# Kernel optimization log

Measured on AMD Instinct MI355X. Metric: run time of the kernel, lower is better.

## Reference

```python
import jax, jax.numpy as jnp
import numpy as np

EPS = 1e-5

def _bn_relu_over_batch(x, gamma, beta):
    # x: [..., B, F] where batch axis is -2; per-step training-mode BatchNorm1d
    mu = x.mean(axis=-2, keepdims=True)
    var = ((x - mu) ** 2).mean(axis=-2, keepdims=True)  # biased var (torch BN)
    xn = (x - mu) * jax.lax.rsqrt(var + EPS)
    return jax.nn.relu(xn * gamma + beta)

def setup_inputs() -> dict:
    key = jax.random.key(0)
    ks = jax.random.split(key, 8)
    B, T, D_in, E, C, D_out = 8192, 128, 2, 128, 128, 5
    s = 0.1
    return {
        "inputs": jax.random.normal(ks[0], (B, T, D_in), jnp.float32),
        "W_emb": jax.random.normal(ks[1], (E, D_in), jnp.float32) * s,
        "b_emb": jnp.zeros((E,), jnp.float32),
        "g_emb": jnp.ones((E,), jnp.float32),
        "be_emb": jnp.zeros((E,), jnp.float32),
        "W_ih": jax.random.normal(ks[2], (4 * C, E), jnp.float32) * s,
        "W_hh": jax.random.normal(ks[3], (4 * C, C), jnp.float32) * s,
        "b_ih": jnp.zeros((4 * C,), jnp.float32),
        "b_hh": jnp.zeros((4 * C,), jnp.float32),
        "W_out": jax.random.normal(ks[4], (D_out, C), jnp.float32) * s,
        "b_out": jnp.zeros((D_out,), jnp.float32),
        "g_out": jnp.ones((D_out,), jnp.float32),
        "be_out": jnp.zeros((D_out,), jnp.float32),
    }

def reference(inputs, W_emb, b_emb, g_emb, be_emb, W_ih, W_hh, b_ih, b_hh,
              W_out, b_out, g_out, be_out):
    B, T, _ = inputs.shape
    C = W_hh.shape[1]
    # Input embedding: Linear + per-step BatchNorm (batch stats) + ReLU, vectorized over T
    x = jnp.einsum('btd,ed->bte', inputs, W_emb) + b_emb      # [B,T,E]
    x = jnp.transpose(x, (1, 0, 2))                           # [T,B,E]
    x = _bn_relu_over_batch(x, g_emb, be_emb)                 # BN over batch per step

    def step(carry, xt):
        h, c = carry
        gates = xt @ W_ih.T + b_ih + h @ W_hh.T + b_hh        # [B,4C]
        i, f, g, o = jnp.split(gates, 4, axis=-1)             # torch LSTMCell order
        i = jax.nn.sigmoid(i); f = jax.nn.sigmoid(f)
        g = jnp.tanh(g); o = jax.nn.sigmoid(o)
        c = f * c + i * g
        h = o * jnp.tanh(c)
        return (h, c), h

    h0 = jnp.zeros((B, C), inputs.dtype)
    _, h_all = jax.lax.scan(step, (h0, h0), x)                # [T,B,C]

    # Output embedding: Linear + per-step BatchNorm + ReLU
    y = jnp.einsum('tbc,oc->tbo', h_all, W_out) + b_out       # [T,B,5]
    y = _bn_relu_over_batch(y, g_out, be_out)
    return jnp.transpose(y, (1, 0, 2))                        # [B,T,5]
```

## Files before the change

### kernel.cpp

```cpp
#include <hip/hip_runtime.h>

typedef __attribute__((ext_vector_type(8))) short short8;
typedef __attribute__((ext_vector_type(4))) float floatx4;

#define B_TOT 8192
#define T_STEPS 128
#define E_DIM 128
#define C_DIM 128
#define D_OUT 5
#define BN_EPS 1e-5f

#define WS_FLAG   0u
#define WS_WCAT   256u
#define WS_WOUT   (WS_WCAT + 262144u)
#define WS_A0     (WS_WOUT + 4096u)
#define WS_A1     (WS_A0 + 65536u)
#define WS_CC     (WS_A1 + 65536u)
#define WS_STATS  (WS_CC + 65536u)
#define WS_Y      (WS_STATS + 5120u)

__device__ __forceinline__ float bf2f(unsigned short h){
  return __uint_as_float(((unsigned int)h) << 16);
}
__device__ __forceinline__ unsigned short f2b(float v){
  unsigned int u = __float_as_uint(v);
  u += 0x7FFFu + ((u >> 16) & 1u);
  return (unsigned short)(u >> 16);
}
__device__ __forceinline__ float ldf(const void* p, int i, int bf){
  return bf ? bf2f(((const unsigned short*)p)[i]) : ((const float*)p)[i];
}
__device__ __forceinline__ float fast_sig(float x){
  float e = __builtin_amdgcn_exp2f(-1.4426950408889634f * x);
  return __builtin_amdgcn_rcpf(1.0f + e);
}
__device__ __forceinline__ float fast_tanh(float x){
  float e = __builtin_amdgcn_exp2f(2.8853900817779268f * x);
  return 1.0f - 2.0f * __builtin_amdgcn_rcpf(1.0f + e);
}

__global__ void k_detect(const void* g_emb, int* flag){
  if (threadIdx.x == 0 && blockIdx.x == 0){
    unsigned int u = *(const unsigned int*)g_emb;
    *flag = (u == 0x3F803F80u) ? 1 : 0;
  }
}

__global__ void k_prep(const void* W_ih, const void* W_hh, const void* W_out,
                       unsigned short* wcat, unsigned short* wout, const int* flagp){
  const int bf = *flagp;
  int i = blockIdx.x * 256 + threadIdx.x;
  if (i < 512*256){
    int n = i >> 8, k = i & 255;
    float v = (k < 128) ? ldf(W_ih, n*128 + k, bf) : ldf(W_hh, n*128 + (k-128), bf);
    wcat[i] = f2b(v);
  } else {
    int j = i - 512*256;
    int n = j >> 7, k = j & 127;
    float v = (n < D_OUT) ? ldf(W_out, n*128 + k, bf) : 0.0f;
    wout[j] = f2b(v);
  }
}

__global__ void k_instats(const void* x, const void* W_emb, const void* g_emb, const void* be_emb,
                          float* A0, float* A1, float* Cc, const int* flagp){
  const int bf = *flagp;
  const int t = blockIdx.x, tid = threadIdx.x;
  float s0=0,s1=0,s00=0,s11=0,s01=0;
  for (int b = tid; b < B_TOT; b += 256){
    int base = (b*T_STEPS + t)*2;
    float x0 = ldf(x, base, bf), x1 = ldf(x, base+1, bf);
    s0+=x0; s1+=x1; s00+=x0*x0; s11+=x1*x1; s01+=x0*x1;
  }
  for (int off = 32; off; off >>= 1){
    s0 += __shfl_down(s0, off, 64); s1 += __shfl_down(s1, off, 64);
    s00 += __shfl_down(s00, off, 64); s11 += __shfl_down(s11, off, 64);
    s01 += __shfl_down(s01, off, 64);
  }
  __shared__ float red[4][5];
  int wid = tid >> 6, lane = tid & 63;
  if (lane == 0){ red[wid][0]=s0; red[wid][1]=s1; red[wid][2]=s00; red[wid][3]=s11; red[wid][4]=s01; }
  __syncthreads();
  if (tid < E_DIM){
    float S0 = red[0][0]+red[1][0]+red[2][0]+red[3][0];
    float S1 = red[0][1]+red[1][1]+red[2][1]+red[3][1];
    float S00= red[0][2]+red[1][2]+red[2][2]+red[3][2];
    float S11= red[0][3]+red[1][3]+red[2][3]+red[3][3];
    float S01= red[0][4]+red[1][4]+red[2][4]+red[3][4];
    const float inv = 1.0f / (float)B_TOT;
    float mu0 = S0*inv, mu1 = S1*inv;
    float v00 = S00*inv - mu0*mu0, v11 = S11*inv - mu1*mu1, c01 = S01*inv - mu0*mu1;
    int e = tid;
    float w0 = ldf(W_emb, e*2, bf), w1 = ldf(W_emb, e*2+1, bf);
    float g  = ldf(g_emb, e, bf),  be = ldf(be_emb, e, bf);
    float var = w0*w0*v00 + 2.0f*w0*w1*c01 + w1*w1*v11;
    float rs = rsqrtf(var + BN_EPS);
    float a0 = g*rs*w0, a1 = g*rs*w1;
    A0[t*E_DIM+e] = a0; A1[t*E_DIM+e] = a1;
    Cc[t*E_DIM+e] = be - (a0*mu0 + a1*mu1);
  }
}

__global__ __launch_bounds__(512, 2)
void k_lstm(const void* x, const void* b_ih, const void* b_hh,
            const unsigned short* __restrict__ wcat, const unsigned short* __restrict__ wout,
            const float* __restrict__ A0, const float* __restrict__ A1, const float* __restrict__ Cc,
            float* __restrict__ y_ws, const int* flagp){
  const int bf = *flagp;
  const int tid = threadIdx.x;
  const int wid = tid >> 6, lane = tid & 63;
  const int q = lane >> 4, s = lane & 15;
  const int row0 = blockIdx.x * 32;

  __shared__ unsigned short xh[2][32][264];

  short8 bfr[4][8];
#pragma unroll
  for (int gq = 0; gq < 4; ++gq)
#pragma unroll
    for (int ks = 0; ks < 8; ++ks)
      bfr[gq][ks] = *(const short8*)(wcat + ((wid + 8*gq)*16 + s)*256 + ks*32 + q*8);

  short8 wf[4];
#pragma unroll
  for (int ks = 0; ks < 4; ++ks)
    wf[ks] = *(const short8*)(wout + s*128 + ks*32 + q*8);

  const int ch = 16*wid + s;
  float bias[4];
#pragma unroll
  for (int gq = 0; gq < 4; ++gq)
    bias[gq] = ldf(b_ih, gq*128 + ch, bf) + ldf(b_hh, gq*128 + ch, bf);

  float c_st[2][4] = {{0,0,0,0},{0,0,0,0}};

  const int r_loc = tid >> 4;
  const int e0 = (tid & 15) * 8;

  auto compute_xe = [&](int tt, int buf){
    float x0, x1;
    int xbase = ((row0 + r_loc)*T_STEPS + tt)*2;
    if (bf){ const unsigned short* xp = (const unsigned short*)x;
      x0 = bf2f(xp[xbase]); x1 = bf2f(xp[xbase+1]);
    } else { const float* xp = (const float*)x; x0 = xp[xbase]; x1 = xp[xbase+1]; }
    floatx4 a0a = *(const floatx4*)(A0 + tt*E_DIM + e0);
    floatx4 a0b = *(const floatx4*)(A0 + tt*E_DIM + e0 + 4);
    floatx4 a1a = *(const floatx4*)(A1 + tt*E_DIM + e0);
    floatx4 a1b = *(const floatx4*)(A1 + tt*E_DIM + e0 + 4);
    floatx4 cca = *(const floatx4*)(Cc + tt*E_DIM + e0);
    floatx4 ccb = *(const floatx4*)(Cc + tt*E_DIM + e0 + 4);
    short8 pack;
#pragma unroll
    for (int j = 0; j < 4; ++j){
      float v  = fmaxf(fmaf(a0a[j], x0, fmaf(a1a[j], x1, cca[j])), 0.0f);
      float v2 = fmaxf(fmaf(a0b[j], x0, fmaf(a1b[j], x1, ccb[j])), 0.0f);
      pack[j]   = (short)f2b(v);
      pack[4+j] = (short)f2b(v2);
    }
    *(short8*)&xh[buf][r_loc][e0] = pack;
  };

  compute_xe(0, 0);
  {
    short8 z; 
#pragma unroll
    for (int j = 0; j < 8; ++j) z[j] = 0;
    *(short8*)&xh[0][r_loc][128 + e0] = z;
  }
  __syncthreads();

  for (int t = 0; t < T_STEPS; ++t){
    const int cb = t & 1, nb = cb ^ 1;

    if (wid < 2 && t > 0){
      floatx4 ya = {0,0,0,0};
#pragma unroll
      for (int ks = 0; ks < 4; ++ks){
        short8 a = *(const short8*)&xh[cb][s + 16*wid][128 + ks*32 + q*8];
        ya = __builtin_amdgcn_mfma_f32_16x16x32_bf16(a, wf[ks], ya, 0, 0, 0);
      }
      if (s < D_OUT){
#pragma unroll
        for (int r = 0; r < 4; ++r){
          int row = row0 + 16*wid + q*4 + r;
          y_ws[((t-1)*B_TOT + row)*D_OUT + s] = ya[r];
        }
      }
    }

    floatx4 acc[2][4];
#pragma unroll
    for (int mt = 0; mt < 2; ++mt)
#pragma unroll
      for (int gq = 0; gq < 4; ++gq) acc[mt][gq] = (floatx4){0,0,0,0};
#pragma unroll
    for (int ks = 0; ks < 8; ++ks){
      short8 a0 = *(const short8*)&xh[cb][s][ks*32 + q*8];
      short8 a1 = *(const short8*)&xh[cb][s + 16][ks*32 + q*8];
#pragma unroll
      for (int gq = 0; gq < 4; ++gq){
        acc[0][gq] = __builtin_amdgcn_mfma_f32_16x16x32_bf16(a0, bfr[gq][ks], acc[0][gq], 0, 0, 0);
        acc[1][gq] = __builtin_amdgcn_mfma_f32_16x16x32_bf16(a1, bfr[gq][ks], acc[1][gq], 0, 0, 0);
      }
    }

#pragma unroll
    for (int mt = 0; mt < 2; ++mt){
#pragma unroll
      for (int r = 0; r < 4; ++r){
        float gi = fast_sig (acc[mt][0][r] + bias[0]);
        float gf = fast_sig (acc[mt][1][r] + bias[1]);
        float gg = fast_tanh(acc[mt][2][r] + bias[2]);
        float go = fast_sig (acc[mt][3][r] + bias[3]);
        float cn = gf * c_st[mt][r] + gi * gg;
        c_st[mt][r] = cn;
        float hv = go * fast_tanh(cn);
        xh[nb][16*mt + q*4 + r][128 + ch] = f2b(hv);
      }
    }

    if (t < T_STEPS-1) compute_xe(t+1, nb);
    __syncthreads();
  }

  if (wid < 2){
    floatx4 ya = {0,0,0,0};
#pragma unroll
    for (int ks = 0; ks < 4; ++ks){
      short8 a = *(const short8*)&xh[0][s + 16*wid][128 + ks*32 + q*8];
      ya = __builtin_amdgcn_mfma_f32_16x16x32_bf16(a, wf[ks], ya, 0, 0, 0);
    }
    if (s < D_OUT){
#pragma unroll
      for (int r = 0; r < 4; ++r){
        int row = row0 + 16*wid + q*4 + r;
        y_ws[((T_STEPS-1)*B_TOT + row)*D_OUT + s] = ya[r];
      }
    }
  }
}

__global__ void k_outstats(const float* __restrict__ y_ws, const void* g_out, const void* be_out,
                           float* stats, const int* flagp){
  const int bf = *flagp;
  const int t = blockIdx.x / 5, o = blockIdx.x % 5;
  const int tid = threadIdx.x;
  float s = 0.0f, ss = 0.0f;
  for (int b = tid; b < B_TOT; b += 256){
    float v = y_ws[(t*B_TOT + b)*D_OUT + o];
    s += v; ss += v*v;
  }
  for (int off = 32; off; off >>= 1){ s += __shfl_down(s, off, 64); ss += __shfl_down(ss, off, 64); }
  __shared__ float red[4][2];
  int wid = tid >> 6, lane = tid & 63;
  if (lane == 0){ red[wid][0] = s; red[wid][1] = ss; }
  __syncthreads();
  if (tid == 0){
    float S  = red[0][0]+red[1][0]+red[2][0]+red[3][0];
    float SS = red[0][1]+red[1][1]+red[2][1]+red[3][1];
    const float inv = 1.0f / (float)B_TOT;
    float mu = S*inv, var = SS*inv - mu*mu;
    float g = ldf(g_out, o, bf), be = ldf(be_out, o, bf);
    float sc = g * rsqrtf(var + BN_EPS);
    stats[blockIdx.x*2]   = sc;
    stats[blockIdx.x*2+1] = be - sc*mu;
  }
}

__global__ void k_apply(const float* __restrict__ y_ws, const float* __restrict__ stats,
                        void* out, const int* flagp){
  const int bf = *flagp;
  int i = blockIdx.x*512 + threadIdx.x;
  int b = i / 640;
  int rem = i - b*640;
  int t = rem / 5, o = rem - t*5;
  float v = y_ws[(t*B_TOT + b)*D_OUT + o];
  int si = (t*5 + o)*2;
  v = fmaxf(fmaf(v, stats[si], stats[si+1]), 0.0f);
  if (bf) ((unsigned short*)out)[i] = f2b(v);
  else    ((float*)out)[i] = v;
}

extern "C" void kernel_launch(void* const* d_in, const int* in_sizes, int n_in,
                              void* d_out, int out_size, void* d_ws, size_t ws_size,
                              hipStream_t stream){
  const void* x      = d_in[0];
  const void* W_emb  = d_in[1];
  const void* g_emb  = d_in[3];
  const void* be_emb = d_in[4];
  const void* W_ih   = d_in[5];
  const void* W_hh   = d_in[6];
  const void* b_ih   = d_in[7];
  const void* b_hh   = d_in[8];
  const void* W_out  = d_in[9];
  const void* g_out  = d_in[11];
  const void* be_out = d_in[12];

  char* ws = (char*)d_ws;
  int* flag = (int*)(ws + WS_FLAG);
  unsigned short* wcat = (unsigned short*)(ws + WS_WCAT);
  unsigned short* wout = (unsigned short*)(ws + WS_WOUT);
  float* A0    = (float*)(ws + WS_A0);
  float* A1    = (float*)(ws + WS_A1);
  float* Cc    = (float*)(ws + WS_CC);
  float* stats = (float*)(ws + WS_STATS);
  float* y_ws  = (float*)(ws + WS_Y);

  k_detect  <<<dim3(1),     dim3(64),  0, stream>>>(g_emb, flag);
  k_prep    <<<dim3(520),   dim3(256), 0, stream>>>(W_ih, W_hh, W_out, wcat, wout, flag);
  k_instats <<<dim3(128),   dim3(256), 0, stream>>>(x, W_emb, g_emb, be_emb, A0, A1, Cc, flag);
  k_lstm    <<<dim3(256),   dim3(512), 0, stream>>>(x, b_ih, b_hh, wcat, wout, A0, A1, Cc, y_ws, flag);
  k_outstats<<<dim3(640),   dim3(256), 0, stream>>>(y_ws, g_out, be_out, stats, flag);
  k_apply   <<<dim3(10240), dim3(512), 0, stream>>>(y_ws, stats, d_out, flag);
}
```

Baseline: 466.9 us.

## Coalesce stats and output kernels, prefetch embedding loads, fold bias into accumulators

The input-statistics kernel is split into a coalesced partial-moments kernel and a small coefficient kernel. The output-statistics kernel now reads each timestep's contiguous block once with LDS atomics. The apply kernel transposes through an LDS tile so global reads and writes are coalesced. Inside the LSTM it prefetches the next step's embedding inputs before the MFMAs, folds the gate bias into the accumulator init, uses cheaper bf16 rounding, pads LDS rows and uses a raw waitcnt+barrier, which adds register pressure and slightly changes rounding.

Result: slower. 487.2 us (+4.3%).

```diff
diff --git a/kernel.cpp b/kernel.cpp
--- a/kernel.cpp
+++ b/kernel.cpp
@@ -17,7 +17,8 @@
 #define WS_A1     (WS_A0 + 65536u)
 #define WS_CC     (WS_A1 + 65536u)
 #define WS_STATS  (WS_CC + 65536u)
-#define WS_Y      (WS_STATS + 5120u)
+#define WS_PART   (WS_STATS + 5120u)
+#define WS_Y      (WS_PART + 20480u)
 
 __device__ __forceinline__ float bf2f(unsigned short h){
   return __uint_as_float(((unsigned int)h) << 16);
@@ -27,6 +28,9 @@
   u += 0x7FFFu + ((u >> 16) & 1u);
   return (unsigned short)(u >> 16);
 }
+__device__ __forceinline__ unsigned short f2b_fast(float v){
+  return (unsigned short)((__float_as_uint(v) + 0x8000u) >> 16);
+}
 __device__ __forceinline__ float ldf(const void* p, int i, int bf){
   return bf ? bf2f(((const unsigned short*)p)[i]) : ((const float*)p)[i];
 }
@@ -37,6 +41,9 @@
 __device__ __forceinline__ float fast_tanh(float x){
   float e = __builtin_amdgcn_exp2f(2.8853900817779268f * x);
   return 1.0f - 2.0f * __builtin_amdgcn_rcpf(1.0f + e);
+}
+__device__ __forceinline__ void lds_barrier(){
+  asm volatile("s_waitcnt lgkmcnt(0)\n\ts_barrier" ::: "memory");
 }
 
 __global__ void k_detect(const void* g_emb, int* flag){
@@ -62,43 +69,88 @@
   }
 }
 
-__global__ void k_instats(const void* x, const void* W_emb, const void* g_emb, const void* be_emb,
-                          float* A0, float* A1, float* Cc, const int* flagp){
-  const int bf = *flagp;
-  const int t = blockIdx.x, tid = threadIdx.x;
-  float s0=0,s1=0,s00=0,s11=0,s01=0;
-  for (int b = tid; b < B_TOT; b += 256){
-    int base = (b*T_STEPS + t)*2;
-    float x0 = ldf(x, base, bf), x1 = ldf(x, base+1, bf);
-    s0+=x0; s1+=x1; s00+=x0*x0; s11+=x1*x1; s01+=x0*x1;
-  }
-  for (int off = 32; off; off >>= 1){
-    s0 += __shfl_down(s0, off, 64); s1 += __shfl_down(s1, off, 64);
-    s00 += __shfl_down(s00, off, 64); s11 += __shfl_down(s11, off, 64);
-    s01 += __shfl_down(s01, off, 64);
-  }
-  __shared__ float red[4][5];
-  int wid = tid >> 6, lane = tid & 63;
-  if (lane == 0){ red[wid][0]=s0; red[wid][1]=s1; red[wid][2]=s00; red[wid][3]=s11; red[wid][4]=s01; }
+__global__ void k_moments(const void* x, float* part, const int* flagp){
+  const int bf = *flagp;
+  const int wdw = (blockIdx.x >> 3) * 8;
+  const int rg  = blockIdx.x & 7;
+  const int tid = threadIdx.x;
+  const int wv = tid >> 6, lane = tid & 63;
+  __shared__ float red[8][16][3];
+
+  if (!bf){
+    const float* xp = (const float*)x;
+    const int row_b = tid >> 4, j = tid & 15;
+    float a0=0, a1=0, a2=0;
+    for (int c = 0; c < 32; ++c){
+      int row = rg*1024 + c*32 + row_b;
+      float v = xp[row*256 + wdw*2 + j];
+      float p = __shfl_xor(v, 1, 64);
+      if ((j & 1) == 0){ a0 += v; a1 += v*v; a2 += v*p; }
+      else             { a0 += v; a1 += v*v; }
+    }
+    a0 += __shfl_down(a0,32,64); a0 += __shfl_down(a0,16,64);
+    a1 += __shfl_down(a1,32,64); a1 += __shfl_down(a1,16,64);
+    a2 += __shfl_down(a2,32,64); a2 += __shfl_down(a2,16,64);
+    if (lane < 16){ red[wv][lane][0]=a0; red[wv][lane][1]=a1; red[wv][lane][2]=a2; }
+  } else {
+    const unsigned int* xp = (const unsigned int*)x;
+    const int row_b = tid >> 3, j = tid & 7;
+    float s0=0,s1=0,s00=0,s11=0,s01=0;
+    for (int c = 0; c < 16; ++c){
+      int row = rg*1024 + c*64 + row_b;
+      unsigned int u = xp[row*128 + wdw + j];
+      float xv0 = bf2f((unsigned short)(u & 0xFFFFu));
+      float xv1 = bf2f((unsigned short)(u >> 16));
+      s0+=xv0; s1+=xv1; s00+=xv0*xv0; s11+=xv1*xv1; s01+=xv0*xv1;
+    }
+    s0 += __shfl_down(s0,32,64); s0 += __shfl_down(s0,16,64); s0 += __shfl_down(s0,8,64);
+    s1 += __shfl_down(s1,32,64); s1 += __shfl_down(s1,16,64); s1 += __shfl_down(s1,8,64);
+    s00+= __shfl_down(s00,32,64);s00+= __shfl_down(s00,16,64);s00+= __shfl_down(s00,8,64);
+    s11+= __shfl_down(s11,32,64);s11+= __shfl_down(s11,16,64);s11+= __shfl_down(s11,8,64);
+    s01+= __shfl_down(s01,32,64);s01+= __shfl_down(s01,16,64);s01+= __shfl_down(s01,8,64);
+    if (lane < 8){
+      red[wv][lane][0]=s0;  red[wv][lane][1]=s00; red[wv][lane][2]=s01;
+      red[wv][8+lane][0]=s1; red[wv][8+lane][1]=s11;
+    }
+  }
   __syncthreads();
-  if (tid < E_DIM){
-    float S0 = red[0][0]+red[1][0]+red[2][0]+red[3][0];
-    float S1 = red[0][1]+red[1][1]+red[2][1]+red[3][1];
-    float S00= red[0][2]+red[1][2]+red[2][2]+red[3][2];
-    float S11= red[0][3]+red[1][3]+red[2][3]+red[3][3];
-    float S01= red[0][4]+red[1][4]+red[2][4]+red[3][4];
-    const float inv = 1.0f / (float)B_TOT;
-    float mu0 = S0*inv, mu1 = S1*inv;
-    float v00 = S00*inv - mu0*mu0, v11 = S11*inv - mu1*mu1, c01 = S01*inv - mu0*mu1;
-    int e = tid;
-    float w0 = ldf(W_emb, e*2, bf), w1 = ldf(W_emb, e*2+1, bf);
-    float g  = ldf(g_emb, e, bf),  be = ldf(be_emb, e, bf);
-    float var = w0*w0*v00 + 2.0f*w0*w1*c01 + w1*w1*v11;
-    float rs = rsqrtf(var + BN_EPS);
-    float a0 = g*rs*w0, a1 = g*rs*w1;
-    A0[t*E_DIM+e] = a0; A1[t*E_DIM+e] = a1;
-    Cc[t*E_DIM+e] = be - (a0*mu0 + a1*mu1);
-  }
+  if (tid < 8){
+    int tl = tid;
+    float S0=0,S1=0,S00=0,S11=0,S01=0;
+    for (int w8 = 0; w8 < 8; ++w8){
+      if (!bf){
+        S0 += red[w8][2*tl][0];   S00 += red[w8][2*tl][1];   S01 += red[w8][2*tl][2];
+        S1 += red[w8][2*tl+1][0]; S11 += red[w8][2*tl+1][1];
+      } else {
+        S0 += red[w8][tl][0];     S00 += red[w8][tl][1];     S01 += red[w8][tl][2];
+        S1 += red[w8][8+tl][0];   S11 += red[w8][8+tl][1];
+      }
+    }
+    float* dst = part + rg*640 + (wdw + tl)*5;
+    dst[0]=S0; dst[1]=S1; dst[2]=S00; dst[3]=S11; dst[4]=S01;
+  }
+}
+
+__global__ void k_coef(const float* part, const void* W_emb, const void* g_emb, const void* be_emb,
+                       float* A0, float* A1, float* Cc, const int* flagp){
+  const int bf = *flagp;
+  int i = blockIdx.x*256 + threadIdx.x;
+  int t = i >> 7, e = i & 127;
+  float S0=0,S1=0,S00=0,S11=0,S01=0;
+  for (int rg = 0; rg < 8; ++rg){
+    const float* p = part + rg*640 + t*5;
+    S0+=p[0]; S1+=p[1]; S00+=p[2]; S11+=p[3]; S01+=p[4];
+  }
+  const float inv = 1.0f / (float)B_TOT;
+  float mu0 = S0*inv, mu1 = S1*inv;
+  float v00 = S00*inv - mu0*mu0, v11 = S11*inv - mu1*mu1, c01 = S01*inv - mu0*mu1;
+  float w0 = ldf(W_emb, e*2, bf), w1 = ldf(W_emb, e*2+1, bf);
+  float g  = ldf(g_emb, e, bf),  be = ldf(be_emb, e, bf);
+  float var = w0*w0*v00 + 2.0f*w0*w1*c01 + w1*w1*v11;
+  float rs = rsqrtf(var + BN_EPS);
+  float a0 = g*rs*w0, a1 = g*rs*w1;
+  A0[i] = a0; A1[i] = a1;
+  Cc[i] = be - (a0*mu0 + a1*mu1);
 }
 
 __global__ __launch_bounds__(512, 2)
@@ -112,7 +164,7 @@
   const int q = lane >> 4, s = lane & 15;
   const int row0 = blockIdx.x * 32;
 
-  __shared__ unsigned short xh[2][32][264];
+  __shared__ unsigned short xh[2][32][266];
 
   short8 bfr[4][8];
 #pragma unroll
@@ -127,50 +179,58 @@
     wf[ks] = *(const short8*)(wout + s*128 + ks*32 + q*8);
 
   const int ch = 16*wid + s;
-  float bias[4];
-#pragma unroll
-  for (int gq = 0; gq < 4; ++gq)
-    bias[gq] = ldf(b_ih, gq*128 + ch, bf) + ldf(b_hh, gq*128 + ch, bf);
+  floatx4 binit[4];
+#pragma unroll
+  for (int gq = 0; gq < 4; ++gq){
+    float b = ldf(b_ih, gq*128 + ch, bf) + ldf(b_hh, gq*128 + ch, bf);
+    binit[gq] = (floatx4){b, b, b, b};
+  }
 
   float c_st[2][4] = {{0,0,0,0},{0,0,0,0}};
 
   const int r_loc = tid >> 4;
   const int e0 = (tid & 15) * 8;
 
-  auto compute_xe = [&](int tt, int buf){
-    float x0, x1;
+  float x0p, x1p;
+  floatx4 pA0a, pA0b, pA1a, pA1b, pCa, pCb;
+
+  auto xe_load = [&](int tt){
     int xbase = ((row0 + r_loc)*T_STEPS + tt)*2;
     if (bf){ const unsigned short* xp = (const unsigned short*)x;
-      x0 = bf2f(xp[xbase]); x1 = bf2f(xp[xbase+1]);
-    } else { const float* xp = (const float*)x; x0 = xp[xbase]; x1 = xp[xbase+1]; }
-    floatx4 a0a = *(const floatx4*)(A0 + tt*E_DIM + e0);
-    floatx4 a0b = *(const floatx4*)(A0 + tt*E_DIM + e0 + 4);
-    floatx4 a1a = *(const floatx4*)(A1 + tt*E_DIM + e0);
-    floatx4 a1b = *(const floatx4*)(A1 + tt*E_DIM + e0 + 4);
-    floatx4 cca = *(const floatx4*)(Cc + tt*E_DIM + e0);
-    floatx4 ccb = *(const floatx4*)(Cc + tt*E_DIM + e0 + 4);
+      x0p = bf2f(xp[xbase]); x1p = bf2f(xp[xbase+1]);
+    } else { const float* xp = (const float*)x; x0p = xp[xbase]; x1p = xp[xbase+1]; }
+    pA0a = *(const floatx4*)(A0 + tt*E_DIM + e0);
+    pA0b = *(const floatx4*)(A0 + tt*E_DIM + e0 + 4);
+    pA1a = *(const floatx4*)(A1 + tt*E_DIM + e0);
+    pA1b = *(const floatx4*)(A1 + tt*E_DIM + e0 + 4);
+    pCa  = *(const floatx4*)(Cc + tt*E_DIM + e0);
+    pCb  = *(const floatx4*)(Cc + tt*E_DIM + e0 + 4);
+  };
+  auto xe_store = [&](int buf){
     short8 pack;
 #pragma unroll
     for (int j = 0; j < 4; ++j){
-      float v  = fmaxf(fmaf(a0a[j], x0, fmaf(a1a[j], x1, cca[j])), 0.0f);
-      float v2 = fmaxf(fmaf(a0b[j], x0, fmaf(a1b[j], x1, ccb[j])), 0.0f);
-      pack[j]   = (short)f2b(v);
-      pack[4+j] = (short)f2b(v2);
+      float v  = fmaxf(fmaf(pA0a[j], x0p, fmaf(pA1a[j], x1p, pCa[j])), 0.0f);
+      float v2 = fmaxf(fmaf(pA0b[j], x0p, fmaf(pA1b[j], x1p, pCb[j])), 0.0f);
+      pack[j]   = (short)f2b_fast(v);
+      pack[4+j] = (short)f2b_fast(v2);
     }
     *(short8*)&xh[buf][r_loc][e0] = pack;
   };
 
-  compute_xe(0, 0);
+  xe_load(0); xe_store(0);
   {
-    short8 z; 
+    short8 z;
 #pragma unroll
     for (int j = 0; j < 8; ++j) z[j] = 0;
     *(short8*)&xh[0][r_loc][128 + e0] = z;
   }
-  __syncthreads();
+  lds_barrier();
 
   for (int t = 0; t < T_STEPS; ++t){
     const int cb = t & 1, nb = cb ^ 1;
+
+    if (t < T_STEPS-1) xe_load(t+1);
 
     if (wid < 2 && t > 0){
       floatx4 ya = {0,0,0,0};
@@ -192,7 +252,7 @@
 #pragma unroll
     for (int mt = 0; mt < 2; ++mt)
 #pragma unroll
-      for (int gq = 0; gq < 4; ++gq) acc[mt][gq] = (floatx4){0,0,0,0};
+      for (int gq = 0; gq < 4; ++gq) acc[mt][gq] = binit[gq];
 #pragma unroll
     for (int ks = 0; ks < 8; ++ks){
       short8 a0 = *(const short8*)&xh[cb][s][ks*32 + q*8];
@@ -208,19 +268,19 @@
     for (int mt = 0; mt < 2; ++mt){
 #pragma unroll
       for (int r = 0; r < 4; ++r){
-        float gi = fast_sig (acc[mt][0][r] + bias[0]);
-        float gf = fast_sig (acc[mt][1][r] + bias[1]);
-        float gg = fast_tanh(acc[mt][2][r] + bias[2]);
-        float go = fast_sig (acc[mt][3][r] + bias[3]);
+        float gi = fast_sig (acc[mt][0][r]);
+        float gf = fast_sig (acc[mt][1][r]);
+        float gg = fast_tanh(acc[mt][2][r]);
+        float go = fast_sig (acc[mt][3][r]);
         float cn = gf * c_st[mt][r] + gi * gg;
         c_st[mt][r] = cn;
         float hv = go * fast_tanh(cn);
-        xh[nb][16*mt + q*4 + r][128 + ch] = f2b(hv);
-      }
-    }
-
-    if (t < T_STEPS-1) compute_xe(t+1, nb);
-    __syncthreads();
+        xh[nb][16*mt + q*4 + r][128 + ch] = f2b_fast(hv);
+      }
+    }
+
+    if (t < T_STEPS-1) xe_store(nb);
+    lds_barrier();
   }
 
   if (wid < 2){
@@ -243,42 +303,56 @@
 __global__ void k_outstats(const float* __restrict__ y_ws, const void* g_out, const void* be_out,
                            float* stats, const int* flagp){
   const int bf = *flagp;
-  const int t = blockIdx.x / 5, o = blockIdx.x % 5;
-  const int tid = threadIdx.x;
-  float s = 0.0f, ss = 0.0f;
-  for (int b = tid; b < B_TOT; b += 256){
-    float v = y_ws[(t*B_TOT + b)*D_OUT + o];
-    s += v; ss += v*v;
-  }
-  for (int off = 32; off; off >>= 1){ s += __shfl_down(s, off, 64); ss += __shfl_down(ss, off, 64); }
-  __shared__ float red[4][2];
-  int wid = tid >> 6, lane = tid & 63;
-  if (lane == 0){ red[wid][0] = s; red[wid][1] = ss; }
+  const int t = blockIdx.x, tid = threadIdx.x;
+  __shared__ float acc2[5][2];
+  if (tid < 10) ((float*)acc2)[tid] = 0.0f;
   __syncthreads();
-  if (tid == 0){
-    float S  = red[0][0]+red[1][0]+red[2][0]+red[3][0];
-    float SS = red[0][1]+red[1][1]+red[2][1]+red[3][1];
+  float s[5] = {0,0,0,0,0}, ss[5] = {0,0,0,0,0};
+  const float* base = y_ws + (size_t)t * 40960;
+#pragma unroll 5
+  for (int it = 0; it < 160; ++it){
+    float v = base[it*256 + tid];
+    s[it % 5] += v; ss[it % 5] += v*v;
+  }
+  int ob = tid % 5;
+#pragma unroll
+  for (int p = 0; p < 5; ++p){
+    int o = ob + p; if (o >= 5) o -= 5;
+    atomicAdd(&acc2[o][0], s[p]);
+    atomicAdd(&acc2[o][1], ss[p]);
+  }
+  __syncthreads();
+  if (tid < 5){
+    float S = acc2[tid][0], SS = acc2[tid][1];
     const float inv = 1.0f / (float)B_TOT;
     float mu = S*inv, var = SS*inv - mu*mu;
-    float g = ldf(g_out, o, bf), be = ldf(be_out, o, bf);
+    float g = ldf(g_out, tid, bf), be = ldf(be_out, tid, bf);
     float sc = g * rsqrtf(var + BN_EPS);
-    stats[blockIdx.x*2]   = sc;
-    stats[blockIdx.x*2+1] = be - sc*mu;
+    stats[(t*5+tid)*2]   = sc;
+    stats[(t*5+tid)*2+1] = be - sc*mu;
   }
 }
 
 __global__ void k_apply(const float* __restrict__ y_ws, const float* __restrict__ stats,
                         void* out, const int* flagp){
   const int bf = *flagp;
-  int i = blockIdx.x*512 + threadIdx.x;
-  int b = i / 640;
-  int rem = i - b*640;
-  int t = rem / 5, o = rem - t*5;
-  float v = y_ws[(t*B_TOT + b)*D_OUT + o];
-  int si = (t*5 + o)*2;
-  v = fmaxf(fmaf(v, stats[si], stats[si+1]), 0.0f);
-  if (bf) ((unsigned short*)out)[i] = f2b(v);
-  else    ((float*)out)[i] = v;
+  __shared__ float tile[128*85];
+  const int b0 = blockIdx.x * 16;
+  const int tid = threadIdx.x;
+  for (int i = tid; i < 10240; i += 256){
+    int t = i / 80, j = i - t*80;
+    tile[t*85 + j] = y_ws[((size_t)t*B_TOT + b0)*D_OUT + j];
+  }
+  __syncthreads();
+  for (int i = tid; i < 10240; i += 256){
+    int b = i / 640, r = i - b*640;
+    int t = r / 5, o = r - t*5;
+    float v = tile[t*85 + b*5 + o];
+    v = fmaxf(fmaf(v, stats[r*2], stats[r*2+1]), 0.0f);
+    int oi = b0*640 + i;
+    if (bf) ((unsigned short*)out)[oi] = f2b(v);
+    else    ((float*)out)[oi] = v;
+  }
 }
 
 extern "C" void kernel_launch(void* const* d_in, const int* in_sizes, int n_in,
@@ -304,12 +378,14 @@
   float* A1    = (float*)(ws + WS_A1);
   float* Cc    = (float*)(ws + WS_CC);
   float* stats = (float*)(ws + WS_STATS);
+  float* part  = (float*)(ws + WS_PART);
   float* y_ws  = (float*)(ws + WS_Y);
 
-  k_detect  <<<dim3(1),     dim3(64),  0, stream>>>(g_emb, flag);
-  k_prep    <<<dim3(520),   dim3(256), 0, stream>>>(W_ih, W_hh, W_out, wcat, wout, flag);
-  k_instats <<<dim3(128),   dim3(256), 0, stream>>>(x, W_emb, g_emb, be_emb, A0, A1, Cc, flag);
-  k_lstm    <<<dim3(256),   dim3(512), 0, stream>>>(x, b_ih, b_hh, wcat, wout, A0, A1, Cc, y_ws, flag);
-  k_outstats<<<dim3(640),   dim3(256), 0, stream>>>(y_ws, g_out, be_out, stats, flag);
-  k_apply   <<<dim3(10240), dim3(512), 0, stream>>>(y_ws, stats, d_out, flag);
-}
+  k_detect  <<<dim3(1),    dim3(64),  0, stream>>>(g_emb, flag);
+  k_prep    <<<dim3(520),  dim3(256), 0, stream>>>(W_ih, W_hh, W_out, wcat, wout, flag);
+  k_moments <<<dim3(128),  dim3(512), 0, stream>>>(x, part, flag);
+  k_coef    <<<dim3(64),   dim3(256), 0, stream>>>(part, W_emb, g_emb, be_emb, A0, A1, Cc, flag);
+  k_lstm    <<<dim3(256),  dim3(512), 0, stream>>>(x, b_ih, b_hh, wcat, wout, A0, A1, Cc, y_ws, flag);
+  k_outstats<<<dim3(128),  dim3(256), 0, stream>>>(y_ws, g_out, be_out, stats, flag);
+  k_apply   <<<dim3(512),  dim3(256), 0, stream>>>(y_ws, stats, d_out, flag);
+}
```
